# Kernel optimization log

Measured on AMD Instinct MI355X. Metric: run time of the kernel, lower is better.

The kernel has to match this reference:

```python
import jax, jax.numpy as jnp
import numpy as np

N_ITER = 4
D = 768  # word_emb_dim == sent_dim of both CrossAttentionBlocks


def setup_inputs() -> dict:
    key = jax.random.key(0)
    ks = jax.random.split(key, 6)
    N_S, N_F = 16384, 4096
    return {
        "sents_emb": jax.random.normal(ks[0], (N_S, D), jnp.float32),
        "func_embed": jax.random.normal(ks[1], (N_F, D), jnp.float32),
        "Wv_f2s": jax.random.normal(ks[2], (D, D), jnp.float32) * 0.02,
        "bv_f2s": jax.random.normal(ks[3], (D,), jnp.float32) * 0.02,
        "Wv_s2f": jax.random.normal(ks[4], (D, D), jnp.float32) * 0.02,
        "bv_s2f": jax.random.normal(ks[5], (D,), jnp.float32) * 0.02,
    }


def reference(sents_emb, func_embed, Wv_f2s, bv_f2s, Wv_s2f, bv_s2f):
    scale = 1.0 / jnp.sqrt(jnp.asarray(D, sents_emb.dtype))
    sents_hid, func_hid = sents_emb, func_embed
    z = None
    for _ in range(N_ITER):  # small fixed iteration count, sequential dependency
        # func2sent: query=sents_hid, key=func_hid, value=W_v(func_hid)
        func_val = func_hid @ Wv_f2s.T + bv_f2s              # [N_f, D]
        z = scale * (sents_hid @ func_hid.T)                  # [N_s, N_f] logits (returned)
        att = jax.nn.softmax(z, axis=1)
        sents_hid = sents_hid + att @ func_val                # [N_s, D]
        # sent2func: query=func_hid, key=sents_hid, value=W_v(sents_hid)
        sent_val = sents_hid @ Wv_s2f.T + bv_s2f              # [N_s, D]
        z2 = scale * (func_hid @ sents_hid.T)                 # [N_f, N_s]
        func_hid = func_hid + jax.nn.softmax(z2, axis=1) @ sent_val
    return (sents_hid, func_hid, z)
```

## Files before the change

### kernel.cpp

```cpp
#include <hip/hip_runtime.h>
#include <stdint.h>

typedef __attribute__((ext_vector_type(8))) short s16x8;
typedef __attribute__((ext_vector_type(8))) unsigned short u16x8;
typedef __attribute__((ext_vector_type(4))) unsigned short u16x4;
typedef __attribute__((ext_vector_type(4))) float f32x4;

__device__ inline unsigned short f2b(float f){
  unsigned u = __builtin_bit_cast(unsigned, f);
  u = u + 0x7fffu + ((u >> 16) & 1u);
  return (unsigned short)(u >> 16);
}
__device__ inline float b2f(unsigned short h){
  unsigned u = ((unsigned)h) << 16;
  return __builtin_bit_cast(float, u);
}

typedef __attribute__((address_space(1))) const unsigned g_uint;
typedef __attribute__((address_space(3))) unsigned l_uint;

__device__ inline void gload_lds16(const void* g, void* l){
  __builtin_amdgcn_global_load_lds((g_uint*)reinterpret_cast<uintptr_t>(g),
                                   (l_uint*)reinterpret_cast<uintptr_t>(l), 16, 0, 0);
}

#define BARF() { __builtin_amdgcn_s_barrier(); asm volatile("" ::: "memory"); }

template<int EPI>
__global__ __launch_bounds__(512, 2) void gemm256(
    const unsigned short* __restrict__ A, const unsigned short* __restrict__ B,
    int M, int N, int K, float scale,
    float* __restrict__ Cf, unsigned short* __restrict__ Cb)
{
  __shared__ __align__(16) char ldsraw[131072];
  const int tid  = threadIdx.x;
  const int wid  = tid >> 6, lane = tid & 63;
  const int wm   = wid >> 2, wn = wid & 3;

  const unsigned gx = gridDim.x, gy = gridDim.y;
  const unsigned lin = blockIdx.x + gx*blockIdx.y;
  const unsigned q   = (gx*gy) >> 3;
  const unsigned w   = (lin & 7)*q + (lin >> 3);
  const int bm = (w / gx) * 256, bn = (w % gx) * 256;

  const int NT = K >> 6;

  f32x4 acc[8][4] = {};

  auto stageA = [&](int T, int halfm){
    const int kb = T << 6;
    char* ldsb = ldsraw + ((T & 1) << 16) + halfm*16384;
    #pragma unroll
    for (int i = 0; i < 2; ++i){
      const int lr  = i*64 + (tid >> 3);
      const int gtr = halfm*64 + ((lr < 64) ? lr : lr + 64);
      const int sc  = ((tid & 7)*8) ^ ((lr & 7)*8);
      gload_lds16(A + (size_t)(bm + gtr)*K + kb + sc, ldsb + i*8192 + tid*16);
    }
  };
  auto stageB = [&](int T, int halfk){
    const int kb = (T << 6) + halfk*32;
    char* ldsb = ldsraw + ((T & 1) << 16) + 32768 + halfk*16384;
    #pragma unroll
    for (int i = 0; i < 2; ++i){
      const int lr = i*128 + (tid >> 2);
      const int sc = ((tid & 3)*8) ^ ((lr & 3)*8);
      gload_lds16(B + (size_t)(bn + lr)*K + kb + sc, ldsb + i*8192 + tid*16);
    }
  };

  const int fr = lane & 15;
  const int fo = (lane >> 4) << 4;
  const int amask = (fr & 7) << 4;
  const int bmask = (fr & 3) << 4;

  auto rdA = [&](const char* ldsS, int mh, int kk, s16x8* af){
    const char* ab = ldsS + mh*16384;
    #pragma unroll
    for (int mf = 0; mf < 4; ++mf){
      const int r = wm*64 + mf*16 + fr;
      af[mf] = *(const s16x8*)(ab + r*128 + ((kk*64 + fo) ^ amask));
    }
  };
  auto rdB = [&](const char* ldsS, int kk, s16x8* bf){
    const char* bb = ldsS + 32768 + kk*16384;
    #pragma unroll
    for (int nf = 0; nf < 4; ++nf){
      const int r = wn*64 + nf*16 + fr;
      bf[nf] = *(const s16x8*)(bb + r*64 + (fo ^ bmask));
    }
  };

  stageB(0, 0); stageA(0, 0); stageA(0, 1); stageB(0, 1);
  stageB(1, 0); stageA(1, 0);
  asm volatile("s_waitcnt vmcnt(4)" ::: "memory");
  BARF();

  for (int T = 0; T < NT; ++T){
    const char* ldsS = ldsraw + ((T & 1) << 16);
    s16x8 af[4], bf[4];
    rdA(ldsS, 0, 0, af); rdB(ldsS, 0, bf);
    if (T + 1 < NT) stageA(T + 1, 1);
    BARF();
    __builtin_amdgcn_s_setprio(1);
    #pragma unroll
    for (int mf = 0; mf < 4; ++mf)
      #pragma unroll
      for (int nf = 0; nf < 4; ++nf)
        acc[mf][nf] = __builtin_amdgcn_mfma_f32_16x16x32_bf16(af[mf], bf[nf], acc[mf][nf], 0, 0, 0);
    __builtin_amdgcn_s_setprio(0);
    BARF();
    rdA(ldsS, 1, 0, af);
    if (T + 1 < NT) stageB(T + 1, 1);
    BARF();
    __builtin_amdgcn_s_setprio(1);
    #pragma unroll
    for (int mf = 0; mf < 4; ++mf)
      #pragma unroll
      for (int nf = 0; nf < 4; ++nf)
        acc[4 + mf][nf] = __builtin_amdgcn_mfma_f32_16x16x32_bf16(af[mf], bf[nf], acc[4 + mf][nf], 0, 0, 0);
    __builtin_amdgcn_s_setprio(0);
    BARF();
    rdA(ldsS, 0, 1, af); rdB(ldsS, 1, bf);
    if (T + 2 < NT) stageB(T + 2, 0);
    BARF();
    __builtin_amdgcn_s_setprio(1);
    #pragma unroll
    for (int mf = 0; mf < 4; ++mf)
      #pragma unroll
      for (int nf = 0; nf < 4; ++nf)
        acc[mf][nf] = __builtin_amdgcn_mfma_f32_16x16x32_bf16(af[mf], bf[nf], acc[mf][nf], 0, 0, 0);
    __builtin_amdgcn_s_setprio(0);
    BARF();
    rdA(ldsS, 1, 1, af);
    if (T + 2 < NT) stageA(T + 2, 0);
    BARF();
    __builtin_amdgcn_s_setprio(1);
    #pragma unroll
    for (int mf = 0; mf < 4; ++mf)
      #pragma unroll
      for (int nf = 0; nf < 4; ++nf)
        acc[4 + mf][nf] = __builtin_amdgcn_mfma_f32_16x16x32_bf16(af[mf], bf[nf], acc[4 + mf][nf], 0, 0, 0);
    __builtin_amdgcn_s_setprio(0);
    if (T < NT - 2) { asm volatile("s_waitcnt vmcnt(4)" ::: "memory"); }
    else           { asm volatile("s_waitcnt vmcnt(0)" ::: "memory"); }
    BARF();
  }

  const int er0 = bm + wm*128 + ((lane >> 4) << 2);
  const int ec0 = bn + wn*64  + (lane & 15);
  #pragma unroll
  for (int mf = 0; mf < 8; ++mf){
    #pragma unroll
    for (int nf = 0; nf < 4; ++nf){
      #pragma unroll
      for (int j = 0; j < 4; ++j){
        const int row = er0 + mf*16 + j;
        const int col = ec0 + nf*16;
        const size_t idx = (size_t)row * N + col;
        const float v = acc[mf][nf][j];
        if (EPI == 5) Cb[idx] = f2b(__expf(v * scale));
        else { const float zz = v * scale; Cf[idx] = zz; Cb[idx] = f2b(__expf(zz)); }
      }
    }
  }
}

template<int EPI>
__global__ __launch_bounds__(256, 4) void gemm_bt(
    const unsigned short* __restrict__ A, const unsigned short* __restrict__ B,
    int M, int N, int KS, float scale, const float* __restrict__ bias,
    const float* __restrict__ linv,
    float* __restrict__ Cf, unsigned short* __restrict__ Cb)
{
  __shared__ unsigned short As[128*64];
  __shared__ unsigned short Bs[128*64];
  const int tid  = threadIdx.x;
  const int wid  = tid >> 6, lane = tid & 63;
  const int wr   = wid >> 1, wc = wid & 1;

  const unsigned gx = gridDim.x, gy = gridDim.y;
  const unsigned lin = blockIdx.x + gx*(blockIdx.y + gy*blockIdx.z);
  const unsigned q   = (gx*gy*gridDim.z) >> 3;
  const unsigned w   = (lin & 7)*q + (lin >> 3);
  const unsigned bxs = w % gx;
  const unsigned rest = w / gx;
  const unsigned bys = rest % gy;
  const unsigned bzs = rest / gy;

  const int bm   = bys * 128, bn = bxs * 128;
  const int kb   = bzs * KS, ke = kb + KS;

  f32x4 acc[4][4] = {};

  const int l8   = lane >> 3;
  const int scol = ((((lane & 7) << 4) ^ (l8 << 4)) >> 1);
  const int Klead = gridDim.z * KS;

  const unsigned short* Ag[4]; const unsigned short* Bg[4];
  unsigned short* Al[4]; unsigned short* Bl[4];
  #pragma unroll
  for (int i = 0; i < 4; ++i){
    const int row = wid*32 + i*8 + l8;
    Ag[i] = A + (size_t)(bm + row) * Klead + scol;
    Bg[i] = B + (size_t)(bn + row) * Klead + scol;
    Al[i] = As + (wid*4 + i) * 512;
    Bl[i] = Bs + (wid*4 + i) * 512;
  }

  const int fr    = lane & 15;
  const int fk    = (lane >> 4) << 4;
  const int amask = (fr & 7) << 4;

  for (int k0 = kb; k0 < ke; k0 += 64){
    if (k0 != kb) __syncthreads();
    #pragma unroll
    for (int i = 0; i < 4; ++i){
      gload_lds16(Ag[i] + k0, Al[i]);
      gload_lds16(Bg[i] + k0, Bl[i]);
    }
    __syncthreads();
    #pragma unroll
    for (int kk = 0; kk < 2; ++kk){
      s16x8 af[4], bf[4];
      #pragma unroll
      for (int m = 0; m < 4; ++m){
        const int row = (wr << 6) + m*16 + fr;
        const int off = row*128 + (((kk << 6) + fk) ^ amask);
        af[m] = *(const s16x8*)((const char*)As + off);
      }
      #pragma unroll
      for (int n = 0; n < 4; ++n){
        const int row = (wc << 6) + n*16 + fr;
        const int off = row*128 + (((kk << 6) + fk) ^ amask);
        bf[n] = *(const s16x8*)((const char*)Bs + off);
      }
      #pragma unroll
      for (int m = 0; m < 4; ++m)
        #pragma unroll
        for (int n = 0; n < 4; ++n)
          acc[m][n] = __builtin_amdgcn_mfma_f32_16x16x32_bf16(af[m], bf[n], acc[m][n], 0, 0, 0);
    }
  }

  const int gr0 = bm + (wr << 6) + ((lane >> 4) << 2);
  const int gc0 = bn + (wc << 6) + (lane & 15);
  const size_t pbase = (size_t)bzs * M * N;
  #pragma unroll
  for (int m = 0; m < 4; ++m){
    #pragma unroll
    for (int j = 0; j < 4; ++j){
      const int row = gr0 + m*16 + j;
      const float li = (EPI == 7) ? linv[row] : 0.f;
      #pragma unroll
      for (int n = 0; n < 4; ++n){
        const int col = gc0 + n*16;
        const size_t idx = (size_t)row * N + col;
        const float v = acc[m][n][j];
        if      (EPI == 2) Cb[idx] = f2b(v + bias[row]);
        else if (EPI == 4) Cf[pbase + idx] = v;
        else if (EPI == 7){ const float o = Cf[idx] + li * v; Cf[idx] = o; Cb[idx] = f2b(o); }
      }
    }
  }
}

__global__ __launch_bounds__(256) void rowsum_att(const unsigned short* __restrict__ E,
                                                  int C, float* __restrict__ linv)
{
  const int row = blockIdx.x, t = threadIdx.x;
  const int lane = t & 63, wid = t >> 6;
  __shared__ float red[4];
  const u16x8* p = (const u16x8*)(E + (size_t)row * C) + t;
  const int nc = C >> 11;
  float s = 0.f;
  for (int c = 0; c < nc; ++c){
    const u16x8 a = p[c * 256];
    #pragma unroll
    for (int j = 0; j < 8; ++j) s += b2f(a[j]);
  }
  #pragma unroll
  for (int o = 32; o; o >>= 1) s += __shfl_xor(s, o, 64);
  if (lane == 0) red[wid] = s;
  __syncthreads();
  if (t == 0) linv[row] = 1.0f / (red[0] + red[1] + red[2] + red[3]);
}

__global__ __launch_bounds__(256) void reduce_splitk(
    const float* __restrict__ P, int S, size_t stride4,
    const float* __restrict__ linv, int d4,
    float* __restrict__ Cf, unsigned short* __restrict__ Cb, int n4)
{
  const int i = blockIdx.x * 256 + threadIdx.x;
  if (i >= n4) return;
  f32x4 s = {0.f, 0.f, 0.f, 0.f};
  for (int k = 0; k < S; ++k) s += ((const f32x4*)P)[(size_t)k * stride4 + i];
  const float li = linv[i / d4];
  f32x4 r = ((const f32x4*)Cf)[i];
  r += s * li;
  ((f32x4*)Cf)[i] = r;
  u16x4 o;
  o[0] = f2b(r[0]); o[1] = f2b(r[1]); o[2] = f2b(r[2]); o[3] = f2b(r[3]);
  ((u16x4*)Cb)[i] = o;
}

__global__ void cvt8(const float* __restrict__ src, float* __restrict__ dstf,
                     unsigned short* __restrict__ dstb, int n8)
{
  const int i = blockIdx.x * 256 + threadIdx.x;
  if (i >= n8) return;
  const f32x4 a = ((const f32x4*)src)[2*i];
  const f32x4 b = ((const f32x4*)src)[2*i + 1];
  if (dstf){ ((f32x4*)dstf)[2*i] = a; ((f32x4*)dstf)[2*i + 1] = b; }
  u16x8 o;
  o[0]=f2b(a[0]); o[1]=f2b(a[1]); o[2]=f2b(a[2]); o[3]=f2b(a[3]);
  o[4]=f2b(b[0]); o[5]=f2b(b[1]); o[6]=f2b(b[2]); o[7]=f2b(b[3]);
  ((u16x8*)dstb)[i] = o;
}

extern "C" void kernel_launch(void* const* d_in, const int* in_sizes, int n_in,
                              void* d_out, int out_size, void* d_ws, size_t ws_size,
                              hipStream_t stream)
{
  (void)in_sizes; (void)n_in; (void)out_size; (void)ws_size;
  const float* sents = (const float*)d_in[0];
  const float* funcs = (const float*)d_in[1];
  const float* WvA   = (const float*)d_in[2];
  const float* bvA   = (const float*)d_in[3];
  const float* WvB   = (const float*)d_in[4];
  const float* bvB   = (const float*)d_in[5];

  const int NS = 16384, NF = 4096, D = 768;

  float* outS = (float*)d_out;
  float* outF = outS + (size_t)NS * D;
  float* outZ = outF + (size_t)NF * D;

  char* ws = (char*)d_ws;
  unsigned short* att = (unsigned short*)ws;  ws += (size_t)NS * NF * 2;
  unsigned short* z2  = att;
  unsigned short* sb  = (unsigned short*)ws;  ws += (size_t)NS * D * 2;
  unsigned short* fb  = (unsigned short*)ws;  ws += (size_t)NF * D * 2;
  unsigned short* fvT = (unsigned short*)ws;  ws += (size_t)D * NF * 2;
  unsigned short* svT = (unsigned short*)ws;  ws += (size_t)D * NS * 2;
  unsigned short* wA  = (unsigned short*)ws;  ws += (size_t)D * D * 2;
  unsigned short* wB  = (unsigned short*)ws;  ws += (size_t)D * D * 2;
  float* linv = (float*)ws;  ws += (size_t)NS * 4;
  float* Pbuf = (float*)ws;  ws += (size_t)NF * D * 4 * 4;

  const float scale = 0.036084391824351615f;

  cvt8<<<dim3((NS*D/8 + 255)/256), 256, 0, stream>>>(sents, outS, sb, NS*D/8);
  cvt8<<<dim3((NF*D/8 + 255)/256), 256, 0, stream>>>(funcs, outF, fb, NF*D/8);
  cvt8<<<dim3((D*D/8 + 255)/256),  256, 0, stream>>>(WvA, nullptr, wA, D*D/8);
  cvt8<<<dim3((D*D/8 + 255)/256),  256, 0, stream>>>(WvB, nullptr, wB, D*D/8);

  for (int it = 0; it < 4; ++it){
    gemm_bt<2><<<dim3(NF/128, D/128, 1), dim3(256), 0, stream>>>(wA, fb, D, NF, D, 0.f, bvA, nullptr, nullptr, fvT);
    if (it < 3){
      gemm256<5><<<dim3(NF/256, NS/256), dim3(512), 0, stream>>>(sb, fb, NS, NF, D, scale, nullptr, att);
    } else {
      gemm256<6><<<dim3(NF/256, NS/256), dim3(512), 0, stream>>>(sb, fb, NS, NF, D, scale, outZ, att);
    }
    rowsum_att<<<dim3(NS), 256, 0, stream>>>(att, NF, linv);
    gemm_bt<7><<<dim3(D/128, NS/128, 1), dim3(256), 0, stream>>>(att, fvT, NS, D, NF, 0.f, nullptr, linv, outS, sb);
    gemm_bt<2><<<dim3(NS/128, D/128, 1), dim3(256), 0, stream>>>(wB, sb, D, NS, D, 0.f, bvB, nullptr, nullptr, svT);
    gemm256<5><<<dim3(NS/256, NF/256), dim3(512), 0, stream>>>(fb, sb, NF, NS, D, scale, nullptr, z2);
    rowsum_att<<<dim3(NF), 256, 0, stream>>>(z2, NS, linv);
    gemm_bt<4><<<dim3(D/128, NF/128, 4), dim3(256), 0, stream>>>(z2, svT, NF, D, 4096, 0.f, nullptr, nullptr, Pbuf, nullptr);
    reduce_splitk<<<dim3(NF*D/4/256), 256, 0, stream>>>(Pbuf, 4, (size_t)NF*D/4, linv, D/4, outF, fb, NF*D/4);
  }
}
```

Measured before the change: 2.269 ms.

## Fuse softmax row-sum into logits GEMM epilogue and change XCD block swizzle

The exp-logits GEMM epilogue now sums each tile's bf16-rounded exponentials per row, reduces them through wave shuffles and LDS atomics, and adds them into a global row-sum buffer with atomics. This replaces the separate rowsum pass that re-read the whole NSxNF bf16 attention matrix. A small kernel then inverts the sums, and a memset clears the buffer before each GEMM. The XCD swizzle also changes to map whole block rows to the same XCD when the grid allows it, aiming for better L2 reuse. The cost is extra epilogue work and global atomics, and the atomics make the summation order nondeterministic.

```diff
diff --git a/kernel.cpp b/kernel.cpp
--- a/kernel.cpp
+++ b/kernel.cpp
@@ -26,11 +26,22 @@
 
 #define BARF() { __builtin_amdgcn_s_barrier(); asm volatile("" ::: "memory"); }
 
+__device__ inline unsigned xcd_swizzle(unsigned lin, unsigned gx, unsigned gyz){
+  const unsigned tot = gx * gyz;
+  const unsigned q = tot >> 3;
+  if ((gyz & 7) == 0){
+    const unsigned group = lin / gx, inner = lin - group * gx;
+    return (group & 7) * q + (group >> 3) * gx + inner;
+  }
+  return (lin & 7) * q + (lin >> 3);
+}
+
 template<int EPI>
 __global__ __launch_bounds__(512, 2) void gemm256(
     const unsigned short* __restrict__ A, const unsigned short* __restrict__ B,
     int M, int N, int K, float scale,
-    float* __restrict__ Cf, unsigned short* __restrict__ Cb)
+    float* __restrict__ Cf, unsigned short* __restrict__ Cb,
+    float* __restrict__ lsum)
 {
   __shared__ __align__(16) char ldsraw[131072];
   const int tid  = threadIdx.x;
@@ -39,8 +50,7 @@
 
   const unsigned gx = gridDim.x, gy = gridDim.y;
   const unsigned lin = blockIdx.x + gx*blockIdx.y;
-  const unsigned q   = (gx*gy) >> 3;
-  const unsigned w   = (lin & 7)*q + (lin >> 3);
+  const unsigned w   = xcd_swizzle(lin, gx, gy);
   const int bm = (w / gx) * 256, bn = (w % gx) * 256;
 
   const int NT = K >> 6;
@@ -147,10 +157,15 @@
     BARF();
   }
 
+  float* lds_rs = (float*)ldsraw;
+  if (tid < 256) lds_rs[tid] = 0.f;
+  __syncthreads();
+
   const int er0 = bm + wm*128 + ((lane >> 4) << 2);
   const int ec0 = bn + wn*64  + (lane & 15);
   #pragma unroll
   for (int mf = 0; mf < 8; ++mf){
+    float rs[4] = {0.f, 0.f, 0.f, 0.f};
     #pragma unroll
     for (int nf = 0; nf < 4; ++nf){
       #pragma unroll
@@ -159,11 +174,26 @@
         const int col = ec0 + nf*16;
         const size_t idx = (size_t)row * N + col;
         const float v = acc[mf][nf][j];
-        if (EPI == 5) Cb[idx] = f2b(__expf(v * scale));
-        else { const float zz = v * scale; Cf[idx] = zz; Cb[idx] = f2b(__expf(zz)); }
+        unsigned short eb;
+        if (EPI == 5){ eb = f2b(__expf(v * scale)); }
+        else { const float zz = v * scale; Cf[idx] = zz; eb = f2b(__expf(zz)); }
+        Cb[idx] = eb;
+        rs[j] += b2f(eb);
       }
     }
-  }
+    #pragma unroll
+    for (int o = 8; o; o >>= 1){
+      #pragma unroll
+      for (int j = 0; j < 4; ++j) rs[j] += __shfl_xor(rs[j], o, 64);
+    }
+    if ((lane & 15) == 0){
+      const int rbase = wm*128 + mf*16 + ((lane >> 4) << 2);
+      #pragma unroll
+      for (int j = 0; j < 4; ++j) atomicAdd(&lds_rs[rbase + j], rs[j]);
+    }
+  }
+  __syncthreads();
+  if (tid < 256) atomicAdd(&lsum[bm + tid], lds_rs[tid]);
 }
 
 template<int EPI>
@@ -181,8 +211,7 @@
 
   const unsigned gx = gridDim.x, gy = gridDim.y;
   const unsigned lin = blockIdx.x + gx*(blockIdx.y + gy*blockIdx.z);
-  const unsigned q   = (gx*gy*gridDim.z) >> 3;
-  const unsigned w   = (lin & 7)*q + (lin >> 3);
+  const unsigned w   = xcd_swizzle(lin, gx, gy*gridDim.z);
   const unsigned bxs = w % gx;
   const unsigned rest = w / gx;
   const unsigned bys = rest % gy;
@@ -265,25 +294,11 @@
   }
 }
 
-__global__ __launch_bounds__(256) void rowsum_att(const unsigned short* __restrict__ E,
-                                                  int C, float* __restrict__ linv)
-{
-  const int row = blockIdx.x, t = threadIdx.x;
-  const int lane = t & 63, wid = t >> 6;
-  __shared__ float red[4];
-  const u16x8* p = (const u16x8*)(E + (size_t)row * C) + t;
-  const int nc = C >> 11;
-  float s = 0.f;
-  for (int c = 0; c < nc; ++c){
-    const u16x8 a = p[c * 256];
-    #pragma unroll
-    for (int j = 0; j < 8; ++j) s += b2f(a[j]);
-  }
-  #pragma unroll
-  for (int o = 32; o; o >>= 1) s += __shfl_xor(s, o, 64);
-  if (lane == 0) red[wid] = s;
-  __syncthreads();
-  if (t == 0) linv[row] = 1.0f / (red[0] + red[1] + red[2] + red[3]);
+__global__ __launch_bounds__(256) void inv_k(const float* __restrict__ lsum,
+                                             float* __restrict__ linv, int n)
+{
+  const int i = blockIdx.x * 256 + threadIdx.x;
+  if (i < n) linv[i] = 1.0f / lsum[i];
 }
 
 __global__ __launch_bounds__(256) void reduce_splitk(
@@ -345,6 +360,7 @@
   unsigned short* svT = (unsigned short*)ws;  ws += (size_t)D * NS * 2;
   unsigned short* wA  = (unsigned short*)ws;  ws += (size_t)D * D * 2;
   unsigned short* wB  = (unsigned short*)ws;  ws += (size_t)D * D * 2;
+  float* lsum = (float*)ws;  ws += (size_t)NS * 4;
   float* linv = (float*)ws;  ws += (size_t)NS * 4;
   float* Pbuf = (float*)ws;  ws += (size_t)NF * D * 4 * 4;
 
@@ -357,16 +373,18 @@
 
   for (int it = 0; it < 4; ++it){
     gemm_bt<2><<<dim3(NF/128, D/128, 1), dim3(256), 0, stream>>>(wA, fb, D, NF, D, 0.f, bvA, nullptr, nullptr, fvT);
+    hipMemsetAsync(lsum, 0, NS*4, stream);
     if (it < 3){
-      gemm256<5><<<dim3(NF/256, NS/256), dim3(512), 0, stream>>>(sb, fb, NS, NF, D, scale, nullptr, att);
+      gemm256<5><<<dim3(NF/256, NS/256), dim3(512), 0, stream>>>(sb, fb, NS, NF, D, scale, nullptr, att, lsum);
     } else {
-      gemm256<6><<<dim3(NF/256, NS/256), dim3(512), 0, stream>>>(sb, fb, NS, NF, D, scale, outZ, att);
-    }
-    rowsum_att<<<dim3(NS), 256, 0, stream>>>(att, NF, linv);
+      gemm256<6><<<dim3(NF/256, NS/256), dim3(512), 0, stream>>>(sb, fb, NS, NF, D, scale, outZ, att, lsum);
+    }
+    inv_k<<<dim3(NS/256), 256, 0, stream>>>(lsum, linv, NS);
     gemm_bt<7><<<dim3(D/128, NS/128, 1), dim3(256), 0, stream>>>(att, fvT, NS, D, NF, 0.f, nullptr, linv, outS, sb);
     gemm_bt<2><<<dim3(NS/128, D/128, 1), dim3(256), 0, stream>>>(wB, sb, D, NS, D, 0.f, bvB, nullptr, nullptr, svT);
-    gemm256<5><<<dim3(NS/256, NF/256), dim3(512), 0, stream>>>(fb, sb, NF, NS, D, scale, nullptr, z2);
-    rowsum_att<<<dim3(NF), 256, 0, stream>>>(z2, NS, linv);
+    hipMemsetAsync(lsum, 0, NF*4, stream);
+    gemm256<5><<<dim3(NS/256, NF/256), dim3(512), 0, stream>>>(fb, sb, NF, NS, D, scale, nullptr, z2, lsum);
+    inv_k<<<dim3(NF/256), 256, 0, stream>>>(lsum, linv, NF);
     gemm_bt<4><<<dim3(D/128, NF/128, 4), dim3(256), 0, stream>>>(z2, svT, NF, D, 4096, 0.f, nullptr, nullptr, Pbuf, nullptr);
     reduce_splitk<<<dim3(NF*D/4/256), 256, 0, stream>>>(Pbuf, 4, (size_t)NF*D/4, linv, D/4, outF, fb, NF*D/4);
   }
```

Result: slower. 2.504 ms (+10.4%).
